# Kernel tuning notes

Hardware: AMD Instinct MI355X
Metric: run time of the kernel (lower is better)

## Reference

```python
import jax, jax.numpy as jnp
import numpy as np

D, FH, FW = 41, 16, 44          # depth bins (arange(4,45,1)), feat H/W = 256/16, 704/16
NX, NY, NZ = 128, 128, 1        # BEV grid from grid_conf
C_CTX = 64                      # LSS context channels
EPS = 1e-5


def _frustum():
    ds = jnp.arange(4.0, 45.0, 1.0)                 # (D,)
    xs = jnp.linspace(0.0, 703.0, FW)
    ys = jnp.linspace(0.0, 255.0, FH)
    return jnp.stack([
        jnp.broadcast_to(xs[None, None, :], (D, FH, FW)),
        jnp.broadcast_to(ys[None, :, None], (D, FH, FW)),
        jnp.broadcast_to(ds[:, None, None], (D, FH, FW)),
    ], -1)                                           # (D,FH,FW,3)


def _bn(x, g, b, m, v):
    # inference-mode BatchNorm2d, x: (B,C,H,W)
    scale = g / jnp.sqrt(v + EPS)
    return x * scale[None, :, None, None] + (b - m * scale)[None, :, None, None]


def setup_inputs() -> dict:
    key = jax.random.key(0)
    ks = jax.random.split(key, 24)
    B, N = 4, 6
    imgs = jax.random.normal(ks[0], (B, N, 3, 256, 704), jnp.float32)
    eye = jnp.eye(3, dtype=jnp.float32)
    # well-conditioned camera matrices (code takes torch.inverse of these)
    rots = eye + 0.05 * jax.random.normal(ks[1], (B, N, 3, 3), jnp.float32)
    trans = 2.0 * jax.random.normal(ks[2], (B, N, 3), jnp.float32)
    K = jnp.array([[500., 0., 352.], [0., 500., 128.], [0., 0., 1.]], jnp.float32)
    kmask = jnp.array([[1., 0., 1.], [0., 1., 1.], [0., 0., 0.]], jnp.float32)
    intrins = K + 5.0 * jax.random.normal(ks[3], (B, N, 3, 3), jnp.float32) * kmask
    post_rots = eye + 0.01 * jax.random.normal(ks[4], (B, N, 3, 3), jnp.float32)
    post_trans = jax.random.normal(ks[5], (B, N, 3), jnp.float32)
    # backbone: Conv2d(3,256,16,16) + BN(256)
    conv_w = 0.02 * jax.random.normal(ks[6], (256, 3, 16, 16), jnp.float32)
    conv_b = 0.01 * jax.random.normal(ks[7], (256,), jnp.float32)
    bn1_g = 1.0 + 0.1 * jax.random.normal(ks[8], (256,), jnp.float32)
    bn1_b = 0.1 * jax.random.normal(ks[9], (256,), jnp.float32)
    bn1_m = 0.1 * jax.random.normal(ks[10], (256,), jnp.float32)
    bn1_v = jax.random.uniform(ks[11], (256,), jnp.float32, 0.5, 1.5)
    # depth_net: Conv2d(256, D+64=105, 1)
    depth_w = 0.05 * jax.random.normal(ks[12], (D + C_CTX, 256), jnp.float32)
    depth_b = 0.01 * jax.random.normal(ks[13], (D + C_CTX,), jnp.float32)
    # BEV encoder: Conv2d(128,64,3,pad=1) + BN(64)
    enc_w = 0.05 * jax.random.normal(ks[14], (64, 128, 3, 3), jnp.float32)
    enc_b = 0.01 * jax.random.normal(ks[15], (64,), jnp.float32)
    bn2_g = 1.0 + 0.1 * jax.random.normal(ks[16], (64,), jnp.float32)
    bn2_b = 0.1 * jax.random.normal(ks[17], (64,), jnp.float32)
    bn2_m = 0.1 * jax.random.normal(ks[18], (64,), jnp.float32)
    bn2_v = jax.random.uniform(ks[19], (64,), jnp.float32, 0.5, 1.5)
    # head: Conv2d(64, 7, 1)
    head_w = 0.05 * jax.random.normal(ks[20], (7, 64), jnp.float32)
    head_b = 0.01 * jax.random.normal(ks[21], (7,), jnp.float32)
    return dict(curr_imgs=imgs, rots=rots, trans=trans, intrins=intrins,
                post_rots=post_rots, post_trans=post_trans,
                conv_w=conv_w, conv_b=conv_b, bn1_g=bn1_g, bn1_b=bn1_b,
                bn1_m=bn1_m, bn1_v=bn1_v, depth_w=depth_w, depth_b=depth_b,
                enc_w=enc_w, enc_b=enc_b, bn2_g=bn2_g, bn2_b=bn2_b,
                bn2_m=bn2_m, bn2_v=bn2_v, head_w=head_w, head_b=head_b)


def _forward(curr_imgs, rots, trans, intrins, post_rots, post_trans,
             conv_w, conv_b, bn1_g, bn1_b, bn1_m, bn1_v,
             depth_w, depth_b, enc_w, enc_b, bn2_g, bn2_b, bn2_m, bn2_v,
             head_w, head_b):
    B, N = curr_imgs.shape[:2]
    dn = ('NCHW', 'OIHW', 'NCHW')
    # backbone (patchify conv + BN + ReLU)
    x = curr_imgs.reshape(B * N, 3, 256, 704)
    x = jax.lax.conv_general_dilated(x, conv_w, (16, 16), 'VALID', dimension_numbers=dn)
    x = jax.nn.relu(_bn(x + conv_b[None, :, None, None], bn1_g, bn1_b, bn1_m, bn1_v))  # (BN,256,16,44)
    # depth net (1x1 conv) -> depth softmax + context
    y = jnp.einsum('oc,bchw->bohw', depth_w, x) + depth_b[None, :, None, None]
    depth = jax.nn.softmax(y[:, :D], axis=1)                 # (BN,D,H,W)
    ctx = y[:, D:]                                           # (BN,C,H,W)
    # LSS outer product: (BN,C,D,H,W) -> (B,N,D,H,W,C)
    outer = ctx[:, :, None] * depth[:, None]
    outer = outer.reshape(B, N, C_CTX, D, FH, FW).transpose(0, 1, 3, 4, 5, 2)
    # geometry: pixel frustum -> ego coords
    fr = _frustum()                                          # (D,FH,FW,3)
    pts = fr[None, None] - post_trans[:, :, None, None, None, :]
    pts = jnp.einsum('bnij,bndhwj->bndhwi', jnp.linalg.inv(post_rots), pts)
    pts = jnp.concatenate([pts[..., :2] * pts[..., 2:3], pts[..., 2:3]], -1)
    comb = rots @ jnp.linalg.inv(intrins)
    pts = jnp.einsum('bnij,bndhwj->bndhwi', comb, pts) + trans[:, :, None, None, None, :]
    # voxel pooling (segment-sum == sort+cumsum trick of the original)
    dx = jnp.array([0.8, 0.8, 20.0], jnp.float32)
    low = jnp.array([-51.2, -51.2, -10.0], jnp.float32)      # bx - dx/2
    coords = ((pts.reshape(-1, 3) - low) / dx).astype(jnp.int32)  # trunc-to-zero like .long()
    rank = coords[:, 0] + coords[:, 1] * NX + coords[:, 2] * NX * NY
    tot = NX * NY * NZ
    kept = (rank >= 0) & (rank < tot)                        # combined-rank check only (as in source)
    feats = outer.reshape(-1, C_CTX) * kept[:, None].astype(outer.dtype)
    bev_flat = jax.ops.segment_sum(feats, jnp.where(kept, rank, 0), num_segments=tot)
    bev = bev_flat.reshape(NZ, NY, NX, C_CTX).transpose(0, 3, 1, 2)  # (1,64,128,128); batch mixed as in source
    # temporal fusion (prev_bev=None branch): cat(bev, bev)
    feat = jnp.concatenate([bev, bev], 1)                    # (1,128,128,128)
    feat = jax.lax.conv_general_dilated(feat, enc_w, (1, 1), 'SAME', dimension_numbers=dn)
    feat = jax.nn.relu(_bn(feat + enc_b[None, :, None, None], bn2_g, bn2_b, bn2_m, bn2_v))
    out = jnp.einsum('oc,bchw->bohw', head_w, feat) + head_b[None, :, None, None]
    return out, bev


def reference(curr_imgs, rots, trans, intrins, post_rots, post_trans,
              conv_w, conv_b, bn1_g, bn1_b, bn1_m, bn1_v,
              depth_w, depth_b, enc_w, enc_b, bn2_g, bn2_b, bn2_m, bn2_v,
              head_w, head_b):
    return _forward(curr_imgs, rots, trans, intrins, post_rots, post_trans,
                    conv_w, conv_b, bn1_g, bn1_b, bn1_m, bn1_v,
                    depth_w, depth_b, enc_w, enc_b, bn2_g, bn2_b, bn2_m, bn2_v,
                    head_w, head_b)
```

## Files before the change

kernel.cpp:

```cpp
#include <hip/hip_runtime.h>
#include <hip/hip_bf16.h>
#include <hip/hip_fp16.h>

#define NPTS 692736
#define NPATCH 16896

typedef _Float16 h16;
typedef __attribute__((ext_vector_type(4))) _Float16 half4v;
typedef __attribute__((ext_vector_type(8))) _Float16 half8v;
typedef __attribute__((ext_vector_type(4))) float f32x4;

__device__ float  v11_xbuf[NPATCH*256];
__device__ float  v11_ctx[NPATCH*64];
__device__ float  v11_depth[NPATCH*41];
__device__ int    v11_ranks[NPTS];
__device__ float  v11_bev[16384*64];
__device__ double v11_geom[24*24];

__device__ h16    v18_whi[196608];
__device__ h16    v18_wlo[196608];

__device__ h16    v15_dwhi[112*256];
__device__ h16    v15_dwlo[112*256];

__device__ h16    v16_w2hi[64*576];
__device__ h16    v16_w2lo[64*576];

__device__ int    v12_cnt[16384];
__device__ int    v12_off[16384];
__device__ int    v12_pos[NPTS];
__device__ int2   v12_sorted[NPTS];
__device__ int    v12_total;

__device__ __forceinline__ void inv3_v11(const double* m, double* o){
  double a=m[0],b=m[1],c=m[2],d=m[3],e=m[4],f=m[5],g=m[6],h=m[7],i=m[8];
  double A = e*i - f*h, B = -(d*i - f*g), C = d*h - e*g;
  double det = a*A + b*B + c*C;
  double id = 1.0/det;
  o[0]=A*id;            o[1]=-(b*i - c*h)*id; o[2]=(b*f - c*e)*id;
  o[3]=B*id;            o[4]=(a*i - c*g)*id;  o[5]=-(a*f - c*d)*id;
  o[6]=C*id;            o[7]=-(a*h - b*g)*id; o[8]=(a*e - b*d)*id;
}

__global__ void zero_v13(){
  int gid = blockIdx.x*256 + threadIdx.x;
  v11_bev[gid] = 0.f;
  if (gid < 16384) v12_cnt[gid] = 0;
}

__global__ void geom_v11(const float* rots, const float* trans, const float* intrins,
                         const float* post_rots, const float* post_trans){
  int t = threadIdx.x;
  if (t >= 24) return;
  double pr[9], it[9], r[9];
  for (int i=0;i<9;i++){
    pr[i] = (double)post_rots[t*9+i];
    it[i] = (double)intrins[t*9+i];
    r[i]  = (double)rots[t*9+i];
  }
  double ipr[9], iit[9];
  inv3_v11(pr, ipr); inv3_v11(it, iit);
  double* g = v11_geom + t*24;
  for (int i=0;i<3;i++) for(int j=0;j<3;j++){
    double s=0; for(int k=0;k<3;k++) s += r[i*3+k]*iit[k*3+j];
    g[9+i*3+j]=s;
  }
  for (int i=0;i<9;i++) g[i]   = ipr[i];
  for (int i=0;i<3;i++) g[18+i]= (double)post_trans[t*3+i];
  for (int i=0;i<3;i++) g[21+i]= (double)trans[t*3+i];
}

__global__ void wt_v18(const float* cw){
  int gid = blockIdx.x*256 + threadIdx.x;
  int e  = gid & 7;
  int t  = gid >> 3;
  int o  = t & 127;
  int t2 = t >> 7;
  int kc = t2 & 7;
  int t3 = t2 >> 3;
  int kt = t3 % 12;
  int ob = t3 / 12;
  int k  = kt*64 + kc*8 + e;
  int oc = ob*128 + o;
  float x = cw[oc*768 + k];
  h16 hi = (h16)x;
  h16 lo = (h16)(x - (float)hi);
  v18_whi[gid] = hi;
  v18_wlo[gid] = lo;
}

__global__ void wtd_v15(const float* dw){
  int gid = blockIdx.x*256 + threadIdx.x;
  int o = gid >> 8, c = gid & 255;
  float x = (o < 105) ? dw[o*256 + c] : 0.f;
  h16 hi = (h16)x;
  h16 lo = (h16)(x - (float)hi);
  v15_dwhi[gid] = hi;
  v15_dwlo[gid] = lo;
}

__global__ void w2_v16(const float* enc_w){
  int gid = blockIdx.x*256 + threadIdx.x;
  if (gid >= 36864) return;
  int o = gid / 576; int k = gid % 576;
  int tap = k >> 6, ic = k & 63;
  float x = enc_w[o*1152 + ic*9 + tap] + enc_w[o*1152 + (ic+64)*9 + tap];
  h16 hi = (h16)x;
  h16 lo = (h16)(x - (float)hi);
  v16_w2hi[gid] = hi;
  v16_w2lo[gid] = lo;
}

__global__ __launch_bounds__(256) void conv1_v19(const float* img,
    const float* cb, const float* g1, const float* b1, const float* m1, const float* v1){
  __shared__ __align__(16) h16 Ah[8][64][8];
  __shared__ __align__(16) h16 Al[8][64][8];
  __shared__ __align__(16) h16 Bh[8192];
  __shared__ __align__(16) h16 Bl[8192];
  int tid  = threadIdx.x;
  int lane = tid & 63, wv = tid >> 6;
  int wr = wv >> 1, wc = wv & 1;
  int pbase = blockIdx.x * 64;

  int pp0 = tid >> 3, kc0 = tid & 7;
  const float* ab[2];
  #pragma unroll
  for (int i=0;i<2;i++){
    int p = pbase + pp0 + 32*i;
    int im = p/704, pix = p%704;
    int ph = pix/44, pw = pix%44;
    ab[i] = img + (size_t)im*540672 + (size_t)ph*16*704 + pw*16;
  }
  const h16* wph = v18_whi + (size_t)blockIdx.y*12*8192;
  const h16* wpl = v18_wlo + (size_t)blockIdx.y*12*8192;

  float4 pa0[2], pa1[2];
  half8v pbh[4], pbl[4];

  auto LOAD_A = [&](int ktI){
    int k0 = ktI*64 + kc0*8;
    int c = k0>>8, rem = k0&255, ky = rem>>4, kx = rem&15;
    size_t goff = (size_t)c*180224 + ky*704 + kx;
    #pragma unroll
    for (int i=0;i<2;i++){
      pa0[i] = *(const float4*)(ab[i] + goff);
      pa1[i] = *(const float4*)(ab[i] + goff + 4);
    }
  };
  auto LOAD_B = [&](int ktI){
    const h16* ph = wph + (size_t)ktI*8192;
    const h16* pl = wpl + (size_t)ktI*8192;
    #pragma unroll
    for (int i=0;i<4;i++){
      int l = tid + i*256;
      pbh[i] = *(const half8v*)(ph + l*8);
      pbl[i] = *(const half8v*)(pl + l*8);
    }
  };

  f32x4 acc[2][4];
  #pragma unroll
  for (int mf=0;mf<2;mf++)
    #pragma unroll
    for (int nf=0;nf<4;nf++) acc[mf][nf] = (f32x4){0.f,0.f,0.f,0.f};

  int fr = lane & 15, fg = lane >> 4;

  LOAD_A(0); LOAD_B(0);

  for (int ktI=0; ktI<12; ktI++){
    __syncthreads();
    #pragma unroll
    for (int i=0;i<2;i++){
      float vv[8] = {pa0[i].x,pa0[i].y,pa0[i].z,pa0[i].w,
                     pa1[i].x,pa1[i].y,pa1[i].z,pa1[i].w};
      half8v hv, lv;
      #pragma unroll
      for (int e=0;e<8;e++){ h16 h=(h16)vv[e]; hv[e]=h; lv[e]=(h16)(vv[e]-(float)h); }
      int srow = (pp0 + 32*i) ^ kc0;
      *(half8v*)&Ah[kc0][srow][0] = hv;
      *(half8v*)&Al[kc0][srow][0] = lv;
    }
    #pragma unroll
    for (int i=0;i<4;i++){
      int l = tid + i*256;
      *(half8v*)&Bh[l*8] = pbh[i];
      *(half8v*)&Bl[l*8] = pbl[i];
    }
    __syncthreads();
    if (ktI < 11){ LOAD_A(ktI+1); LOAD_B(ktI+1); }
    #pragma unroll
    for (int ks=0;ks<2;ks++){
      int kc = ks*4 + fg;
      half8v ah[2], al[2], bh[4], bl[4];
      #pragma unroll
      for (int mf=0;mf<2;mf++){
        int row = (wr*32 + mf*16 + fr) ^ kc;
        ah[mf] = *(const half8v*)&Ah[kc][row][0];
        al[mf] = *(const half8v*)&Al[kc][row][0];
      }
      #pragma unroll
      for (int nf=0;nf<4;nf++){
        int col = wc*64 + nf*16 + fr;
        bh[nf] = *(const half8v*)&Bh[(kc*128 + col)*8];
        bl[nf] = *(const half8v*)&Bl[(kc*128 + col)*8];
      }
      #pragma unroll
      for (int mf=0;mf<2;mf++)
        #pragma unroll
        for (int nf=0;nf<4;nf++){
          acc[mf][nf] = __builtin_amdgcn_mfma_f32_16x16x32_f16(ah[mf], bh[nf], acc[mf][nf], 0,0,0);
          acc[mf][nf] = __builtin_amdgcn_mfma_f32_16x16x32_f16(ah[mf], bl[nf], acc[mf][nf], 0,0,0);
          acc[mf][nf] = __builtin_amdgcn_mfma_f32_16x16x32_f16(al[mf], bh[nf], acc[mf][nf], 0,0,0);
        }
    }
  }
  int obase = blockIdx.y * 128;
  #pragma unroll
  for (int nf=0;nf<4;nf++){
    int ch = obase + wc*64 + nf*16 + fr;
    float sc = g1[ch] / sqrtf(v1[ch] + 1e-5f);
    float sh = b1[ch] - m1[ch]*sc;
    float bi = cb[ch];
    #pragma unroll
    for (int mf=0;mf<2;mf++){
      #pragma unroll
      for (int j=0;j<4;j++){
        int pq = pbase + wr*32 + mf*16 + fg*4 + j;
        float t = (acc[mf][nf][j] + bi)*sc + sh;
        v11_xbuf[(size_t)pq*256 + ch] = t > 0.f ? t : 0.f;
      }
    }
  }
}

__global__ __launch_bounds__(256) void depth_v16(const float* db){
  __shared__ __align__(16) h16 Ah[4][64][8];
  __shared__ __align__(16) h16 Al[4][64][8];
  __shared__ __align__(16) h16 Bh[4][112][8];
  __shared__ __align__(16) h16 Bl[4][112][8];
  __shared__ float sy[64*113];
  int tid = threadIdx.x;
  int lane = tid & 63, wv = tid >> 6;
  int pbase = blockIdx.x*64;
  int fr = lane & 15, fg = lane >> 4;

  int app = tid & 63;
  int kcA = tid >> 6;
  const float* xsrc = &v11_xbuf[(size_t)(pbase+app)*256 + kcA*8];

  f32x4 acc[7];
  #pragma unroll
  for (int nf=0;nf<7;nf++) acc[nf] = (f32x4){0.f,0.f,0.f,0.f};

  for (int kt=0; kt<256; kt+=32){
    __syncthreads();
    {
      float4 v0 = *(const float4*)(xsrc + kt);
      float4 v1 = *(const float4*)(xsrc + kt + 4);
      float vv[8] = {v0.x,v0.y,v0.z,v0.w,v1.x,v1.y,v1.z,v1.w};
      half8v hv, lv;
      #pragma unroll
      for (int e=0;e<8;e++){ h16 h=(h16)vv[e]; hv[e]=h; lv[e]=(h16)(vv[e]-(float)h); }
      *(half8v*)&Ah[kcA][app][0] = hv;
      *(half8v*)&Al[kcA][app][0] = lv;
    }
    for (int l = tid; l < 448; l += 256){
      int kc = l/112, o = l%112;
      *(half8v*)&Bh[kc][o][0] = *(const half8v*)&v15_dwhi[o*256 + kt + kc*8];
      *(half8v*)&Bl[kc][o][0] = *(const half8v*)&v15_dwlo[o*256 + kt + kc*8];
    }
    __syncthreads();
    int row = wv*16 + fr;
    half8v ah = *(const half8v*)&Ah[fg][row][0];
    half8v al = *(const half8v*)&Al[fg][row][0];
    #pragma unroll
    for (int nf=0;nf<7;nf++){
      int col = nf*16 + fr;
      half8v bh = *(const half8v*)&Bh[fg][col][0];
      half8v bl = *(const half8v*)&Bl[fg][col][0];
      acc[nf] = __builtin_amdgcn_mfma_f32_16x16x32_f16(ah, bh, acc[nf], 0,0,0);
      acc[nf] = __builtin_amdgcn_mfma_f32_16x16x32_f16(ah, bl, acc[nf], 0,0,0);
      acc[nf] = __builtin_amdgcn_mfma_f32_16x16x32_f16(al, bh, acc[nf], 0,0,0);
    }
  }
  #pragma unroll
  for (int nf=0;nf<7;nf++){
    int o = nf*16 + fr;
    if (o < 105){
      float bias = db[o];
      #pragma unroll
      for (int j=0;j<4;j++){
        int pp = wv*16 + fg*4 + j;
        sy[pp*113 + o] = acc[nf][j] + bias;
      }
    }
  }
  __syncthreads();
  if (tid < 64){
    float* y = &sy[tid*113];
    float m = y[0];
    for (int i=1;i<41;i++) m = fmaxf(m, y[i]);
    float s = 0.f;
    for (int i=0;i<41;i++){ float e = expf(y[i]-m); y[i] = e; s += e; }
    float inv = 1.f/s;
    for (int i=0;i<41;i++) y[i] *= inv;
  }
  __syncthreads();
  for (int l = tid; l < 64*41; l += 256){
    int pp = l/41, dd = l%41;
    v11_depth[(size_t)(pbase+pp)*41 + dd] = sy[pp*113+dd];
  }
  for (int l = tid; l < 64*64; l += 256){
    int pp = l>>6, c = l&63;
    v11_ctx[(size_t)(pbase+pp)*64 + c] = sy[pp*113 + 41 + c];
  }
}

__global__ __launch_bounds__(256) void rank_v13(){
  __shared__ int lh[16384];
  int tid = threadIdx.x;
  for (int i = tid; i < 16384; i += 256) lh[i] = 0;
  __syncthreads();
  int base = blockIdx.x*1024;
  int rk[4], lp[4];
  #pragma unroll
  for (int k=0;k<4;k++){
    int idx = base + k*256 + tid;
    rk[k] = -1; lp[k] = 0;
    if (idx < NPTS){
      int im = idx / 28864;
      int r  = idx % 28864;
      int d  = r / 704; int pix = r % 704;
      int h = pix / 44, w = pix % 44;
      const double* g = v11_geom + im*24;
      double fx = (double)w * (703.0/43.0);
      double fy = (double)h * 17.0;
      double fz = 4.0 + (double)d;
      double px = fx - g[18], py = fy - g[19], pz = fz - g[20];
      double q0 = g[0]*px + g[1]*py + g[2]*pz;
      double q1 = g[3]*px + g[4]*py + g[5]*pz;
      double q2 = g[6]*px + g[7]*py + g[8]*pz;
      q0 *= q2; q1 *= q2;
      double o0 = g[9]*q0  + g[10]*q1 + g[11]*q2 + g[21];
      double o1 = g[12]*q0 + g[13]*q1 + g[14]*q2 + g[22];
      double o2 = g[15]*q0 + g[16]*q1 + g[17]*q2 + g[23];
      int cx = (int)((o0 + 51.2)/0.8);
      int cy = (int)((o1 + 51.2)/0.8);
      int cz = (int)((o2 + 10.0)/20.0);
      int rank = cx + cy*128 + cz*16384;
      if (rank >= 0 && rank < 16384){
        rk[k] = rank;
        lp[k] = atomicAdd(&lh[rank], 1);
      }
    }
  }
  __syncthreads();
  for (int i = tid; i < 16384; i += 256){
    int h = lh[i];
    if (h) lh[i] = atomicAdd(&v12_cnt[i], h);
  }
  __syncthreads();
  #pragma unroll
  for (int k=0;k<4;k++){
    int idx = base + k*256 + tid;
    if (idx < NPTS){
      v11_ranks[idx] = rk[k];
      if (rk[k] >= 0) v12_pos[idx] = lh[rk[k]] + lp[k];
    }
  }
}

__global__ __launch_bounds__(256) void scan_v13(){
  __shared__ int part[256];
  int t = threadIdx.x;
  int base = t*64;
  int s = 0;
  for (int i=0;i<64;i++) s += v12_cnt[base+i];
  part[t] = s;
  __syncthreads();
  if (t == 0){
    int run = 0;
    for (int i=0;i<256;i++){ int v = part[i]; part[i] = run; run += v; }
    v12_total = run;
  }
  __syncthreads();
  int run = part[t];
  for (int i=0;i<64;i++){
    v12_off[base+i] = run;
    run += v12_cnt[base+i];
  }
}

__global__ __launch_bounds__(256) void fill_v13(){
  int idx = blockIdx.x*256 + threadIdx.x;
  if (idx >= NPTS) return;
  int rank = v11_ranks[idx];
  if (rank < 0) return;
  int im = idx / 28864;
  int r  = idx % 28864;
  int d  = r / 704; int pix = r % 704;
  int p  = im*704 + pix;
  int pos = v12_off[rank] + v12_pos[idx];
  v12_sorted[pos] = make_int2((p<<6) | d, rank);
}

__global__ __launch_bounds__(256) void gather_v13(){
  int total = v12_total;
  int w = threadIdx.x >> 6;
  int chunk = blockIdx.x*256 + w*64;
  if (chunk >= total) return;
  int lane = threadIdx.x & 63;
  int n = total - chunk; if (n > 64) n = 64;
  int pv = 0, rv = -1;
  float dv = 0.f;
  if (lane < n){
    int2 sr = v12_sorted[chunk + lane];
    pv = sr.x; rv = sr.y;
    dv = v11_depth[(pv>>6)*41 + (pv & 63)];
  }
  float acc = 0.f;
  int cur = __shfl(rv, 0);
  for (int i = 0; i < n; i++){
    int rk = __shfl(rv, i);
    int pp = __shfl(pv, i) >> 6;
    float dd = __shfl(dv, i);
    if (rk != cur){
      atomicAdd(&v11_bev[(size_t)cur*64 + lane], acc);
      acc = 0.f; cur = rk;
    }
    acc += v11_ctx[(pp<<6) | lane] * dd;
  }
  atomicAdd(&v11_bev[(size_t)cur*64 + lane], acc);
}

__global__ void bevout_v11(float* out1){
  int gid = blockIdx.x*256 + threadIdx.x;
  int c  = gid >> 14;
  int yx = gid & 16383;
  out1[gid] = v11_bev[(size_t)yx*64 + c];
}

__global__ __launch_bounds__(256) void conv2_v17(
    const float* eb, const float* g2, const float* b2_, const float* m2, const float* v2,
    const float* hw, const float* hb, float* out0){
  __shared__ __align__(16) h16 Ah[4][64][8];
  __shared__ __align__(16) h16 Al[4][64][8];
  __shared__ __align__(16) h16 Bh[4][64][8];
  __shared__ __align__(16) h16 Bl[4][64][8];
  __shared__ float sfeat[64*68];
  __shared__ float hred[4*64*7];
  int tid = threadIdx.x;
  int lane = tid & 63, wv = tid >> 6;
  int bx = blockIdx.x & 15, by = blockIdx.x >> 4;
  int fr = lane & 15, fg = lane >> 4;

  int app = tid & 63;
  int kcT = tid >> 6;
  int apy = app >> 3, apx = app & 7;

  f32x4 acc[4];
  #pragma unroll
  for (int nf=0;nf<4;nf++) acc[nf] = (f32x4){0.f,0.f,0.f,0.f};

  for (int kt=0; kt<576; kt+=32){
    int tap = kt >> 6, ic0 = kt & 32;
    int dy = tap/3 - 1, dx = tap%3 - 1;
    __syncthreads();
    {
      int gy = by*8 + apy + dy, gx = bx*8 + apx + dx;
      float4 v0 = {0.f,0.f,0.f,0.f}, v1 = {0.f,0.f,0.f,0.f};
      if (gy>=0 && gy<128 && gx>=0 && gx<128){
        const float* src = &v11_bev[(size_t)(gy*128+gx)*64 + ic0 + kcT*8];
        v0 = *(const float4*)src;
        v1 = *(const float4*)(src+4);
      }
      float vv[8] = {v0.x,v0.y,v0.z,v0.w,v1.x,v1.y,v1.z,v1.w};
      half8v hv, lv;
      #pragma unroll
      for (int e=0;e<8;e++){ h16 h=(h16)vv[e]; hv[e]=h; lv[e]=(h16)(vv[e]-(float)h); }
      *(half8v*)&Ah[kcT][app][0] = hv;
      *(half8v*)&Al[kcT][app][0] = lv;
    }
    {
      *(half8v*)&Bh[kcT][app][0] = *(const half8v*)&v16_w2hi[app*576 + kt + kcT*8];
      *(half8v*)&Bl[kcT][app][0] = *(const half8v*)&v16_w2lo[app*576 + kt + kcT*8];
    }
    __syncthreads();
    int row = wv*16 + fr;
    half8v ah = *(const half8v*)&Ah[fg][row][0];
    half8v al = *(const half8v*)&Al[fg][row][0];
    #pragma unroll
    for (int nf=0;nf<4;nf++){
      int col = nf*16 + fr;
      half8v bh = *(const half8v*)&Bh[fg][col][0];
      half8v bl = *(const half8v*)&Bl[fg][col][0];
      acc[nf] = __builtin_amdgcn_mfma_f32_16x16x32_f16(ah, bh, acc[nf], 0,0,0);
      acc[nf] = __builtin_amdgcn_mfma_f32_16x16x32_f16(ah, bl, acc[nf], 0,0,0);
      acc[nf] = __builtin_amdgcn_mfma_f32_16x16x32_f16(al, bh, acc[nf], 0,0,0);
    }
  }
  #pragma unroll
  for (int nf=0;nf<4;nf++){
    int ch = nf*16 + fr;
    float sc = g2[ch]/sqrtf(v2[ch]+1e-5f);
    float sh = b2_[ch] - m2[ch]*sc;
    float bi = eb[ch];
    #pragma unroll
    for (int j=0;j<4;j++){
      int pp = wv*16 + fg*4 + j;
      float t = (acc[nf][j] + bi)*sc + sh;
      sfeat[pp*68 + ch] = t > 0.f ? t : 0.f;
    }
  }
  __syncthreads();
  int og = tid >> 6, pix = tid & 63;
  float part[7];
  #pragma unroll
  for (int o=0;o<7;o++) part[o]=0.f;
  #pragma unroll
  for (int j=0;j<16;j++){
    int oc = og*16 + j;
    float v = sfeat[pix*68 + oc];
    #pragma unroll
    for (int o=0;o<7;o++) part[o] += hw[o*64+oc]*v;
  }
  #pragma unroll
  for (int o=0;o<7;o++) hred[(og*64+pix)*7+o] = part[o];
  __syncthreads();
  if (og == 0){
    int gy = by*8 + (pix>>3), gx = bx*8 + (pix&7);
    #pragma unroll
    for (int o=0;o<7;o++){
      float s = hred[pix*7+o] + hred[(64+pix)*7+o] + hred[(128+pix)*7+o]
              + hred[(192+pix)*7+o] + hb[o];
      out0[o*16384 + gy*128 + gx] = s;
    }
  }
}

extern "C" void kernel_launch(void* const* d_in, const int* in_sizes, int n_in,
                              void* d_out, int out_size, void* d_ws, size_t ws_size,
                              hipStream_t stream){
  const float* imgs       = (const float*)d_in[0];
  const float* rots       = (const float*)d_in[1];
  const float* trans      = (const float*)d_in[2];
  const float* intrins    = (const float*)d_in[3];
  const float* post_rots  = (const float*)d_in[4];
  const float* post_trans = (const float*)d_in[5];
  const float* conv_w     = (const float*)d_in[6];
  const float* conv_b     = (const float*)d_in[7];
  const float* bn1_g      = (const float*)d_in[8];
  const float* bn1_b      = (const float*)d_in[9];
  const float* bn1_m      = (const float*)d_in[10];
  const float* bn1_v      = (const float*)d_in[11];
  const float* depth_w    = (const float*)d_in[12];
  const float* depth_b    = (const float*)d_in[13];
  const float* enc_w      = (const float*)d_in[14];
  const float* enc_b      = (const float*)d_in[15];
  const float* bn2_g      = (const float*)d_in[16];
  const float* bn2_b      = (const float*)d_in[17];
  const float* bn2_m      = (const float*)d_in[18];
  const float* bn2_v      = (const float*)d_in[19];
  const float* head_w     = (const float*)d_in[20];
  const float* head_b     = (const float*)d_in[21];

  float* out0 = (float*)d_out;
  float* out1 = out0 + 114688;

  zero_v13<<<4096, 256, 0, stream>>>();
  geom_v11<<<1, 32, 0, stream>>>(rots, trans, intrins, post_rots, post_trans);
  wt_v18<<<768, 256, 0, stream>>>(conv_w);
  wtd_v15<<<112, 256, 0, stream>>>(depth_w);
  w2_v16<<<144, 256, 0, stream>>>(enc_w);
  conv1_v19<<<dim3(264, 2), 256, 0, stream>>>(imgs, conv_b, bn1_g, bn1_b, bn1_m, bn1_v);
  depth_v16<<<264, 256, 0, stream>>>(depth_b);
  rank_v13<<<(NPTS+1023)/1024, 256, 0, stream>>>();
  scan_v13<<<1, 256, 0, stream>>>();
  fill_v13<<<NPTS/256, 256, 0, stream>>>();
  gather_v13<<<NPTS/256, 256, 0, stream>>>();
  bevout_v11<<<4096, 256, 0, stream>>>(out1);
  conv2_v17<<<256, 256, 0, stream>>>(enc_b, bn2_g, bn2_b, bn2_m, bn2_v,
                                     head_w, head_b, out0);
}
```

Before: 265.3 us.

## Merge prep kernels into one launch and halve conv1 output-channel tile

Five small setup kernels (zeroing, geometry, and three weight-splitting passes) become one kernel that dispatches on block index, removing four launches. The conv1 GEMM tile shrinks from 128 to 64 output channels per block, with the weight layout repacked to match. The grid doubles to 264x4 blocks and each block uses fewer registers and less LDS, which should raise occupancy and parallelism on the GPU's many CUs. In exchange, each image patch tile is loaded and converted four times instead of twice.

```diff
diff --git a/kernel.cpp b/kernel.cpp
--- a/kernel.cpp
+++ b/kernel.cpp
@@ -17,8 +17,8 @@
 __device__ float  v11_bev[16384*64];
 __device__ double v11_geom[24*24];
 
-__device__ h16    v18_whi[196608];
-__device__ h16    v18_wlo[196608];
+__device__ h16    v20_whi[196608];
+__device__ h16    v20_wlo[196608];
 
 __device__ h16    v15_dwhi[112*256];
 __device__ h16    v15_dwlo[112*256];
@@ -42,81 +42,76 @@
   o[6]=C*id;            o[7]=-(a*h - b*g)*id; o[8]=(a*e - b*d)*id;
 }
 
-__global__ void zero_v13(){
-  int gid = blockIdx.x*256 + threadIdx.x;
-  v11_bev[gid] = 0.f;
-  if (gid < 16384) v12_cnt[gid] = 0;
-}
-
-__global__ void geom_v11(const float* rots, const float* trans, const float* intrins,
+__global__ void prep_v20(const float* cw, const float* dw, const float* enc_w,
+                         const float* rots, const float* trans, const float* intrins,
                          const float* post_rots, const float* post_trans){
-  int t = threadIdx.x;
-  if (t >= 24) return;
-  double pr[9], it[9], r[9];
-  for (int i=0;i<9;i++){
-    pr[i] = (double)post_rots[t*9+i];
-    it[i] = (double)intrins[t*9+i];
-    r[i]  = (double)rots[t*9+i];
-  }
-  double ipr[9], iit[9];
-  inv3_v11(pr, ipr); inv3_v11(it, iit);
-  double* g = v11_geom + t*24;
-  for (int i=0;i<3;i++) for(int j=0;j<3;j++){
-    double s=0; for(int k=0;k<3;k++) s += r[i*3+k]*iit[k*3+j];
-    g[9+i*3+j]=s;
-  }
-  for (int i=0;i<9;i++) g[i]   = ipr[i];
-  for (int i=0;i<3;i++) g[18+i]= (double)post_trans[t*3+i];
-  for (int i=0;i<3;i++) g[21+i]= (double)trans[t*3+i];
-}
-
-__global__ void wt_v18(const float* cw){
-  int gid = blockIdx.x*256 + threadIdx.x;
-  int e  = gid & 7;
-  int t  = gid >> 3;
-  int o  = t & 127;
-  int t2 = t >> 7;
-  int kc = t2 & 7;
-  int t3 = t2 >> 3;
-  int kt = t3 % 12;
-  int ob = t3 / 12;
-  int k  = kt*64 + kc*8 + e;
-  int oc = ob*128 + o;
-  float x = cw[oc*768 + k];
-  h16 hi = (h16)x;
-  h16 lo = (h16)(x - (float)hi);
-  v18_whi[gid] = hi;
-  v18_wlo[gid] = lo;
-}
-
-__global__ void wtd_v15(const float* dw){
-  int gid = blockIdx.x*256 + threadIdx.x;
-  int o = gid >> 8, c = gid & 255;
-  float x = (o < 105) ? dw[o*256 + c] : 0.f;
-  h16 hi = (h16)x;
-  h16 lo = (h16)(x - (float)hi);
-  v15_dwhi[gid] = hi;
-  v15_dwlo[gid] = lo;
-}
-
-__global__ void w2_v16(const float* enc_w){
-  int gid = blockIdx.x*256 + threadIdx.x;
-  if (gid >= 36864) return;
-  int o = gid / 576; int k = gid % 576;
-  int tap = k >> 6, ic = k & 63;
-  float x = enc_w[o*1152 + ic*9 + tap] + enc_w[o*1152 + (ic+64)*9 + tap];
-  h16 hi = (h16)x;
-  h16 lo = (h16)(x - (float)hi);
-  v16_w2hi[gid] = hi;
-  v16_w2lo[gid] = lo;
-}
-
-__global__ __launch_bounds__(256) void conv1_v19(const float* img,
+  int b = blockIdx.x;
+  int tid = threadIdx.x;
+  if (b < 4096){
+    int gid = b*256 + tid;
+    v11_bev[gid] = 0.f;
+    if (gid < 16384) v12_cnt[gid] = 0;
+  } else if (b < 4864){
+    int gid = (b-4096)*256 + tid;
+    int e  = gid & 7;
+    int t  = gid >> 3;
+    int o  = t & 63;
+    int t2 = t >> 6;
+    int kc = t2 & 7;
+    int t3 = t2 >> 3;
+    int kt = t3 % 12;
+    int ob = t3 / 12;
+    int k  = kt*64 + kc*8 + e;
+    int oc = ob*64 + o;
+    float x = cw[oc*768 + k];
+    h16 hi = (h16)x;
+    v20_whi[gid] = hi;
+    v20_wlo[gid] = (h16)(x - (float)hi);
+  } else if (b < 4976){
+    int gid = (b-4864)*256 + tid;
+    int o = gid >> 8, c = gid & 255;
+    float x = (o < 105) ? dw[o*256 + c] : 0.f;
+    h16 hi = (h16)x;
+    v15_dwhi[gid] = hi;
+    v15_dwlo[gid] = (h16)(x - (float)hi);
+  } else if (b < 5120){
+    int gid = (b-4976)*256 + tid;
+    if (gid < 36864){
+      int o = gid / 576; int k = gid % 576;
+      int tap = k >> 6, ic = k & 63;
+      float x = enc_w[o*1152 + ic*9 + tap] + enc_w[o*1152 + (ic+64)*9 + tap];
+      h16 hi = (h16)x;
+      v16_w2hi[gid] = hi;
+      v16_w2lo[gid] = (h16)(x - (float)hi);
+    }
+  } else {
+    int t = tid;
+    if (t >= 24) return;
+    double pr[9], it[9], r[9];
+    for (int i=0;i<9;i++){
+      pr[i] = (double)post_rots[t*9+i];
+      it[i] = (double)intrins[t*9+i];
+      r[i]  = (double)rots[t*9+i];
+    }
+    double ipr[9], iit[9];
+    inv3_v11(pr, ipr); inv3_v11(it, iit);
+    double* g = v11_geom + t*24;
+    for (int i=0;i<3;i++) for(int j=0;j<3;j++){
+      double s=0; for(int k=0;k<3;k++) s += r[i*3+k]*iit[k*3+j];
+      g[9+i*3+j]=s;
+    }
+    for (int i=0;i<9;i++) g[i]   = ipr[i];
+    for (int i=0;i<3;i++) g[18+i]= (double)post_trans[t*3+i];
+    for (int i=0;i<3;i++) g[21+i]= (double)trans[t*3+i];
+  }
+}
+
+__global__ __launch_bounds__(256) void conv1_v20(const float* img,
     const float* cb, const float* g1, const float* b1, const float* m1, const float* v1){
   __shared__ __align__(16) h16 Ah[8][64][8];
   __shared__ __align__(16) h16 Al[8][64][8];
-  __shared__ __align__(16) h16 Bh[8192];
-  __shared__ __align__(16) h16 Bl[8192];
+  __shared__ __align__(16) h16 Bh[4096];
+  __shared__ __align__(16) h16 Bl[4096];
   int tid  = threadIdx.x;
   int lane = tid & 63, wv = tid >> 6;
   int wr = wv >> 1, wc = wv & 1;
@@ -131,11 +126,11 @@
     int ph = pix/44, pw = pix%44;
     ab[i] = img + (size_t)im*540672 + (size_t)ph*16*704 + pw*16;
   }
-  const h16* wph = v18_whi + (size_t)blockIdx.y*12*8192;
-  const h16* wpl = v18_wlo + (size_t)blockIdx.y*12*8192;
+  const h16* wph = v20_whi + (size_t)blockIdx.y*12*4096;
+  const h16* wpl = v20_wlo + (size_t)blockIdx.y*12*4096;
 
   float4 pa0[2], pa1[2];
-  half8v pbh[4], pbl[4];
+  half8v pbh[2], pbl[2];
 
   auto LOAD_A = [&](int ktI){
     int k0 = ktI*64 + kc0*8;
@@ -148,21 +143,21 @@
     }
   };
   auto LOAD_B = [&](int ktI){
-    const h16* ph = wph + (size_t)ktI*8192;
-    const h16* pl = wpl + (size_t)ktI*8192;
-    #pragma unroll
-    for (int i=0;i<4;i++){
+    const h16* ph = wph + (size_t)ktI*4096;
+    const h16* pl = wpl + (size_t)ktI*4096;
+    #pragma unroll
+    for (int i=0;i<2;i++){
       int l = tid + i*256;
       pbh[i] = *(const half8v*)(ph + l*8);
       pbl[i] = *(const half8v*)(pl + l*8);
     }
   };
 
-  f32x4 acc[2][4];
+  f32x4 acc[2][2];
   #pragma unroll
   for (int mf=0;mf<2;mf++)
     #pragma unroll
-    for (int nf=0;nf<4;nf++) acc[mf][nf] = (f32x4){0.f,0.f,0.f,0.f};
+    for (int nf=0;nf<2;nf++) acc[mf][nf] = (f32x4){0.f,0.f,0.f,0.f};
 
   int fr = lane & 15, fg = lane >> 4;
 
@@ -182,7 +177,7 @@
       *(half8v*)&Al[kc0][srow][0] = lv;
     }
     #pragma unroll
-    for (int i=0;i<4;i++){
+    for (int i=0;i<2;i++){
       int l = tid + i*256;
       *(half8v*)&Bh[l*8] = pbh[i];
       *(half8v*)&Bl[l*8] = pbl[i];
@@ -192,7 +187,7 @@
     #pragma unroll
     for (int ks=0;ks<2;ks++){
       int kc = ks*4 + fg;
-      half8v ah[2], al[2], bh[4], bl[4];
+      half8v ah[2], al[2], bh[2], bl[2];
       #pragma unroll
       for (int mf=0;mf<2;mf++){
         int row = (wr*32 + mf*16 + fr) ^ kc;
@@ -200,25 +195,25 @@
         al[mf] = *(const half8v*)&Al[kc][row][0];
       }
       #pragma unroll
-      for (int nf=0;nf<4;nf++){
-        int col = wc*64 + nf*16 + fr;
-        bh[nf] = *(const half8v*)&Bh[(kc*128 + col)*8];
-        bl[nf] = *(const half8v*)&Bl[(kc*128 + col)*8];
+      for (int nf=0;nf<2;nf++){
+        int col = wc*32 + nf*16 + fr;
+        bh[nf] = *(const half8v*)&Bh[(kc*64 + col)*8];
+        bl[nf] = *(const half8v*)&Bl[(kc*64 + col)*8];
       }
       #pragma unroll
       for (int mf=0;mf<2;mf++)
         #pragma unroll
-        for (int nf=0;nf<4;nf++){
+        for (int nf=0;nf<2;nf++){
           acc[mf][nf] = __builtin_amdgcn_mfma_f32_16x16x32_f16(ah[mf], bh[nf], acc[mf][nf], 0,0,0);
           acc[mf][nf] = __builtin_amdgcn_mfma_f32_16x16x32_f16(ah[mf], bl[nf], acc[mf][nf], 0,0,0);
           acc[mf][nf] = __builtin_amdgcn_mfma_f32_16x16x32_f16(al[mf], bh[nf], acc[mf][nf], 0,0,0);
         }
     }
   }
-  int obase = blockIdx.y * 128;
-  #pragma unroll
-  for (int nf=0;nf<4;nf++){
-    int ch = obase + wc*64 + nf*16 + fr;
+  int obase = blockIdx.y * 64;
+  #pragma unroll
+  for (int nf=0;nf<2;nf++){
+    int ch = obase + wc*32 + nf*16 + fr;
     float sc = g1[ch] / sqrtf(v1[ch] + 1e-5f);
     float sh = b1[ch] - m1[ch]*sc;
     float bi = cb[ch];
@@ -568,12 +563,9 @@
   float* out0 = (float*)d_out;
   float* out1 = out0 + 114688;
 
-  zero_v13<<<4096, 256, 0, stream>>>();
-  geom_v11<<<1, 32, 0, stream>>>(rots, trans, intrins, post_rots, post_trans);
-  wt_v18<<<768, 256, 0, stream>>>(conv_w);
-  wtd_v15<<<112, 256, 0, stream>>>(depth_w);
-  w2_v16<<<144, 256, 0, stream>>>(enc_w);
-  conv1_v19<<<dim3(264, 2), 256, 0, stream>>>(imgs, conv_b, bn1_g, bn1_b, bn1_m, bn1_v);
+  prep_v20<<<5121, 256, 0, stream>>>(conv_w, depth_w, enc_w,
+                                     rots, trans, intrins, post_rots, post_trans);
+  conv1_v20<<<dim3(264, 4), 256, 0, stream>>>(imgs, conv_b, bn1_g, bn1_b, bn1_m, bn1_v);
   depth_v16<<<264, 256, 0, stream>>>(depth_b);
   rank_v13<<<(NPTS+1023)/1024, 256, 0, stream>>>();
   scan_v13<<<1, 256, 0, stream>>>();
```

New measurement: 260.4 us. Within noise of the previous version (-1.8%).
